# Performance work log

Hardware: AMD Instinct MI355X
Metric: run time of the kernel (lower is better)

## Reference

```python
import jax, jax.numpy as jnp
import numpy as np

B, ACT, C, H = 2048, 14, 128, 32
N = B * ACT                      # total nodes
E = B * ACT * ACT                # batched GCN edges
LOG_STD_MIN, LOG_STD_MAX = -20.0, 2.0


def setup_inputs() -> dict:
    key = jax.random.key(0)
    ks = jax.random.split(key, 8)
    def w(k, shape, fan_in):
        return jax.random.normal(k, shape, jnp.float32) / np.sqrt(fan_in).astype(np.float32)
    return {
        "state": jax.random.normal(ks[0], (N, C), jnp.float32),
        "conv_W": w(ks[1], (C, C), C),
        "conv_b": jnp.zeros((C,), jnp.float32),
        "lin1_W": w(ks[2], (2 * C, H), 2 * C),
        "lin1_b": jnp.zeros((H,), jnp.float32),
        "lin2_W": w(ks[3], (H, H), H),
        "lin2_b": jnp.zeros((H,), jnp.float32),
        "mu_W": w(ks[4], (H, 1), H),
        "mu_b": jnp.zeros((1,), jnp.float32),
        "sig_W": w(ks[5], (H, 1), H),
        "sig_b": jnp.zeros((1,), jnp.float32),
        "edge_index": jax.random.randint(ks[6], (2, E), 0, N, jnp.int32),
    }


def gcn_conv(x, W, b, src, dst):
    # PyG GCNConv default: add self-loops + symmetric normalization
    xw = x @ W                                           # [N, C]
    ones = jnp.ones(src.shape, x.dtype)
    deg = jax.ops.segment_sum(ones, dst, num_segments=N) + 1.0   # self-loop included
    dinv = jax.lax.rsqrt(deg)                            # deg^{-1/2}
    norm = dinv[src] * dinv[dst]                         # per-edge weight
    agg = jax.ops.segment_sum(xw[src] * norm[:, None], dst, num_segments=N)
    return agg + xw * (dinv * dinv)[:, None] + b         # self-loop term + bias


def reference(state, conv_W, conv_b, lin1_W, lin1_b, lin2_W, lin2_b,
              mu_W, mu_b, sig_W, sig_b, edge_index):
    src, dst = edge_index[0], edge_index[1]
    out = jax.nn.relu(gcn_conv(state, conv_W, conv_b, src, dst))
    x = (out + state).reshape(B, ACT, C)                 # [B, 14, C]
    # self.edges = all 196 directed pairs (i, j) over the 14-node graph
    e_src = jnp.repeat(jnp.arange(ACT), ACT)             # edges[:, 0]
    e_dst = jnp.tile(jnp.arange(ACT), ACT)               # edges[:, 1]
    ef = jnp.concatenate([x[:, e_src, :], x[:, e_dst, :]], axis=2)  # [B, 196, 2C]
    h = jax.nn.leaky_relu(ef @ lin1_W + lin1_b)          # slope 0.01 (torch default)
    h = jax.nn.leaky_relu(h @ lin2_W + lin2_b)           # [B, 196, H]
    log_std = jnp.clip(h @ sig_W + sig_b, LOG_STD_MIN, LOG_STD_MAX)
    std = jnp.exp(log_std)[..., 0]                       # [B, 196]
    mu = jax.nn.softplus(h @ mu_W + mu_b + 1e-10)[..., 0]  # [B, 196]
    # distribution parameters (return_D / deterministic paths)
    return jnp.stack([mu, std], axis=0)                  # [2, B, 196]
```

## Files before the change

kernel.cpp:

```cpp
#include <hip/hip_runtime.h>
#include <hip/hip_bf16.h>
#include <math.h>

#define NB    2048
#define ACT   14
#define NC    128
#define NH    32
#define NNODE (NB*ACT)
#define NEDGE (NB*ACT*ACT)
#define NPAIR (NB*ACT*ACT)
#define BCAP  64

__device__ __forceinline__ unsigned short f2bf(float f)
{
    unsigned u = __float_as_uint(f);
    return (unsigned short)((u + 0x7fff + ((u >> 16) & 1)) >> 16);
}
__device__ __forceinline__ float bfl(unsigned v) { return __uint_as_float(v << 16); }
__device__ __forceinline__ float bfh(unsigned v) { return __uint_as_float(v & 0xffff0000u); }

__global__ __launch_bounds__(256) void init_misc(
    int* __restrict__ cnt, unsigned short* __restrict__ ydummy,
    const float* __restrict__ W1, float* __restrict__ Wp)
{
    int idx = blockIdx.x * 256 + threadIdx.x;
    if (idx < NNODE) cnt[idx] = 0;
    if (idx < 128) ydummy[idx] = 0;
    if (idx < 128 * 64) {
        int k = idx >> 6, c = idx & 63;
        Wp[idx] = (c < 32) ? W1[k * 32 + c] : W1[(128 + k) * 32 + (c - 32)];
    }
}

__global__ void bucket_fill(const int* __restrict__ src, const int* __restrict__ dst,
                            int* __restrict__ cnt, int* __restrict__ bucket)
{
    int e = blockIdx.x * blockDim.x + threadIdx.x;
    if (e < NEDGE) {
        int d = dst[e];
        int slot = atomicAdd(&cnt[d], 1);
        if (slot < BCAP) bucket[(size_t)d * BCAP + slot] = src[e];
    }
}

__global__ __launch_bounds__(256) void gemm_k128_bf16(
    const float* __restrict__ A, const float* __restrict__ W,
    unsigned short* __restrict__ C, int ncols, const int* __restrict__ cnt)
{
    __shared__ float As[64 * 128];
    __shared__ float Ws[128 * 64];
    const int tid  = threadIdx.x;
    const int row0 = blockIdx.x * 64;
    const int col0 = blockIdx.y * 64;

    {
        const float4* Ag = (const float4*)(A + (size_t)row0 * 128);
#pragma unroll
        for (int it = 0; it < 8; ++it) {
            int idx = tid + it * 256;
            int r = idx >> 5;
            int c = (idx & 31) << 2;
            int cs = c ^ (((r >> 2) & 3) << 2);
            *((float4*)&As[r * 128 + cs]) = Ag[r * 32 + (c >> 2)];
        }
#pragma unroll
        for (int it = 0; it < 8; ++it) {
            int idx = tid + it * 256;
            int k = idx >> 4;
            int c = (idx & 15) << 2;
            *((float4*)&Ws[k * 64 + c]) =
                *((const float4*)&W[(size_t)k * ncols + col0 + c]);
        }
    }
    __syncthreads();

    const int tx = tid & 15;
    const int ty = tid >> 4;
    const int ri0 = ty * 4;

    float acc[4][4] = {};
    for (int k = 0; k < 128; k += 4) {
        float a_s[4][4];
        float w_s[4][4];
#pragma unroll
        for (int i = 0; i < 4; ++i) {
            int r = ri0 + i;
            *((float4*)&a_s[i][0]) =
                *((const float4*)&As[r * 128 + (k ^ (((r >> 2) & 3) << 2))]);
        }
#pragma unroll
        for (int kk = 0; kk < 4; ++kk) {
            *((float4*)&w_s[kk][0]) =
                *((const float4*)&Ws[(k + kk) * 64 + tx * 4]);
        }
#pragma unroll
        for (int kk = 0; kk < 4; ++kk)
#pragma unroll
            for (int i = 0; i < 4; ++i)
#pragma unroll
                for (int j = 0; j < 4; ++j)
                    acc[i][j] += a_s[i][kk] * w_s[kk][j];
    }

#pragma unroll
    for (int i = 0; i < 4; ++i) {
        float s = rsqrtf((float)cnt[row0 + ri0 + i] + 1.0f);
        ushort4 o;
        o.x = f2bf(acc[i][0] * s);
        o.y = f2bf(acc[i][1] * s);
        o.z = f2bf(acc[i][2] * s);
        o.w = f2bf(acc[i][3] * s);
        *((ushort4*)&C[(size_t)(row0 + ri0 + i) * ncols + col0 + tx * 4]) = o;
    }
}

__global__ __launch_bounds__(256) void gemm_k128(
    const float* __restrict__ A, const float* __restrict__ W,
    float* __restrict__ C, int ncols)
{
    __shared__ float As[64 * 128];
    __shared__ float Ws[128 * 64];
    const int tid  = threadIdx.x;
    const int row0 = blockIdx.x * 64;
    const int col0 = blockIdx.y * 64;

    {
        const float4* Ag = (const float4*)(A + (size_t)row0 * 128);
#pragma unroll
        for (int it = 0; it < 8; ++it) {
            int idx = tid + it * 256;
            int r = idx >> 5;
            int c = (idx & 31) << 2;
            int cs = c ^ (((r >> 2) & 3) << 2);
            *((float4*)&As[r * 128 + cs]) = Ag[r * 32 + (c >> 2)];
        }
#pragma unroll
        for (int it = 0; it < 8; ++it) {
            int idx = tid + it * 256;
            int k = idx >> 4;
            int c = (idx & 15) << 2;
            *((float4*)&Ws[k * 64 + c]) =
                *((const float4*)&W[(size_t)k * ncols + col0 + c]);
        }
    }
    __syncthreads();

    const int tx = tid & 15;
    const int ty = tid >> 4;
    const int ri0 = ty * 4;

    float acc[4][4] = {};
    for (int k = 0; k < 128; k += 4) {
        float a_s[4][4];
        float w_s[4][4];
#pragma unroll
        for (int i = 0; i < 4; ++i) {
            int r = ri0 + i;
            *((float4*)&a_s[i][0]) =
                *((const float4*)&As[r * 128 + (k ^ (((r >> 2) & 3) << 2))]);
        }
#pragma unroll
        for (int kk = 0; kk < 4; ++kk) {
            *((float4*)&w_s[kk][0]) =
                *((const float4*)&Ws[(k + kk) * 64 + tx * 4]);
        }
#pragma unroll
        for (int kk = 0; kk < 4; ++kk)
#pragma unroll
            for (int i = 0; i < 4; ++i)
#pragma unroll
                for (int j = 0; j < 4; ++j)
                    acc[i][j] += a_s[i][kk] * w_s[kk][j];
    }

#pragma unroll
    for (int i = 0; i < 4; ++i) {
        float4 v = make_float4(acc[i][0], acc[i][1], acc[i][2], acc[i][3]);
        *((float4*)&C[(size_t)(row0 + ri0 + i) * ncols + col0 + tx * 4]) = v;
    }
}

__global__ __launch_bounds__(256) void gather_agg(
    const int* __restrict__ bucket, const int* __restrict__ cnt,
    const unsigned short* __restrict__ y, const float* __restrict__ bias,
    const float* __restrict__ state, float* __restrict__ xout)
{
    const int lane = threadIdx.x & 31;
    const int d = (blockIdx.x * 256 + threadIdx.x) >> 5;
    if (d >= NNODE) return;

    const int c_true = cnt[d];
    const int c = c_true < BCAP ? c_true : BCAP;

    uint2 sv0 = ((const uint2*)(y + (size_t)d * NC))[lane];
    float4 acc;
    acc.x = bfl(sv0.x); acc.y = bfh(sv0.x);
    acc.z = bfl(sv0.y); acc.w = bfh(sv0.y);

    const int* brow = bucket + (size_t)d * BCAP;
    for (int base = 0; base < c; base += 32) {
        int rem = c - base;
        int m = rem < 32 ? rem : 32;
        int sv = (lane < m) ? brow[base + lane] : NNODE;
        int mm = (m + 3) & ~3;
        for (int j = 0; j < mm; j += 4) {
            int s0 = __shfl(sv, j + 0, 32);
            int s1 = __shfl(sv, j + 1, 32);
            int s2 = __shfl(sv, j + 2, 32);
            int s3 = __shfl(sv, j + 3, 32);
            uint2 a0 = ((const uint2*)(y + (size_t)s0 * NC))[lane];
            uint2 a1 = ((const uint2*)(y + (size_t)s1 * NC))[lane];
            uint2 a2 = ((const uint2*)(y + (size_t)s2 * NC))[lane];
            uint2 a3 = ((const uint2*)(y + (size_t)s3 * NC))[lane];
            acc.x += bfl(a0.x) + bfl(a1.x) + bfl(a2.x) + bfl(a3.x);
            acc.y += bfh(a0.x) + bfh(a1.x) + bfh(a2.x) + bfh(a3.x);
            acc.z += bfl(a0.y) + bfl(a1.y) + bfl(a2.y) + bfl(a3.y);
            acc.w += bfh(a0.y) + bfh(a1.y) + bfh(a2.y) + bfh(a3.y);
        }
    }

    const float dv = rsqrtf((float)c_true + 1.0f);
    float4 b  = ((const float4*)bias)[lane];
    float4 st = ((const float4*)(state + (size_t)d * NC))[lane];
    float4 r;
    r.x = fmaxf(acc.x * dv + b.x, 0.f) + st.x;
    r.y = fmaxf(acc.y * dv + b.y, 0.f) + st.y;
    r.z = fmaxf(acc.z * dv + b.z, 0.f) + st.z;
    r.w = fmaxf(acc.w * dv + b.w, 0.f) + st.w;
    ((float4*)(xout + (size_t)d * NC))[lane] = r;
}

__device__ __forceinline__ float softplusf(float z)
{
    return z > 0.f ? z + log1pf(expf(-z)) : log1pf(expf(z));
}

__global__ __launch_bounds__(256) void pairs_sgpr_kernel(
    const float* __restrict__ uv, const float* __restrict__ W2,
    const float* __restrict__ b1, const float* __restrict__ b2,
    const float* __restrict__ muW, const float* __restrict__ mu_b,
    const float* __restrict__ sigW, const float* __restrict__ sig_b,
    float* __restrict__ out)
{
    const int gid = blockIdx.x * 256 + threadIdx.x;
    const int b = gid / 196;
    const int p = gid - b * 196;
    const int i = p / 14;
    const int j = p - i * 14;

    const float* up = uv + (size_t)(b * ACT + i) * 64;
    const float* vp = uv + (size_t)(b * ACT + j) * 64 + 32;

    float h2[32];
#pragma unroll
    for (int l = 0; l < 32; ++l) h2[l] = b2[l];

#pragma unroll 2
    for (int k4 = 0; k4 < 8; ++k4) {
        float4 uu = ((const float4*)up)[k4];
        float4 vv = ((const float4*)vp)[k4];
#pragma unroll
        for (int kk = 0; kk < 4; ++kk) {
            float uvk = (kk == 0) ? uu.x + vv.x :
                        (kk == 1) ? uu.y + vv.y :
                        (kk == 2) ? uu.z + vv.z : uu.w + vv.w;
            float z = uvk + b1[k4 * 4 + kk];
            float h1k = z > 0.f ? z : 0.01f * z;
            const float* wrow = W2 + (k4 * 4 + kk) * 32;
#pragma unroll
            for (int l = 0; l < 32; ++l)
                h2[l] += h1k * wrow[l];
        }
    }

    float mu_acc = mu_b[0] + 1e-10f;
    float sg = sig_b[0];
#pragma unroll
    for (int l = 0; l < 32; ++l) {
        float h = h2[l];
        h = h > 0.f ? h : 0.01f * h;
        mu_acc += h * muW[l];
        sg += h * sigW[l];
    }
    out[gid]         = softplusf(mu_acc);
    out[NPAIR + gid] = expf(fminf(fmaxf(sg, -20.f), 2.f));
}

extern "C" void kernel_launch(void* const* d_in, const int* in_sizes, int n_in,
                              void* d_out, int out_size, void* d_ws, size_t ws_size,
                              hipStream_t stream)
{
    const float* state  = (const float*)d_in[0];
    const float* conv_W = (const float*)d_in[1];
    const float* conv_b = (const float*)d_in[2];
    const float* lin1_W = (const float*)d_in[3];
    const float* lin1_b = (const float*)d_in[4];
    const float* lin2_W = (const float*)d_in[5];
    const float* lin2_b = (const float*)d_in[6];
    const float* mu_W   = (const float*)d_in[7];
    const float* mu_b   = (const float*)d_in[8];
    const float* sig_W  = (const float*)d_in[9];
    const float* sig_b  = (const float*)d_in[10];
    const int*   eidx   = (const int*)d_in[11];
    const int* e_src = eidx;
    const int* e_dst = eidx + NEDGE;

    float* out = (float*)d_out;

    char* wsb = (char*)d_ws;
    unsigned short* y = (unsigned short*)wsb;
    char* p = wsb + (size_t)(NNODE + 1) * NC * sizeof(unsigned short);
    float* x = (float*)p;            p += (size_t)NNODE * NC * sizeof(float);
    int* cnt = (int*)p;              p += (size_t)NNODE * sizeof(int);
    int* bucket = (int*)p;           p += (size_t)NNODE * BCAP * sizeof(int);
    float* Wp = (float*)p;           p += 128 * 64 * sizeof(float);
    float* uvb = (float*)p;

    init_misc<<<(NNODE + 255) / 256, 256, 0, stream>>>(
        cnt, y + (size_t)NNODE * NC, lin1_W, Wp);

    bucket_fill<<<NEDGE / 256, 256, 0, stream>>>(e_src, e_dst, cnt, bucket);

    gemm_k128_bf16<<<dim3(NNODE / 64, 2), 256, 0, stream>>>(
        state, conv_W, y, 128, cnt);

    gather_agg<<<(NNODE * 32) / 256, 256, 0, stream>>>(
        bucket, cnt, y, conv_b, state, x);

    gemm_k128<<<dim3(NNODE / 64, 1), 256, 0, stream>>>(x, Wp, uvb, 64);

    pairs_sgpr_kernel<<<NPAIR / 256, 256, 0, stream>>>(
        uvb, lin2_W, lin1_b, lin2_b, mu_W, mu_b, sig_W, sig_b, out);
}
```

Baseline: 94.27 us.

## Compute pair-MLP second layer with bf16 MFMA instead of scalar FMAs

The per-pair 32x32 lin2 layer is rewritten so each wave processes 16 pairs with two 16x16x32 bf16 MFMA instructions, using a transposed bf16 copy of lin2_W built in the init kernel. Results go through shared memory, and 16 lanes per wave then finish the bias, leaky-relu and mu/sigma heads. This is meant to remove the heavy scalar FMA work of the old one-pair-per-thread kernel. In exchange, the first-layer activations and the weights are rounded to bf16, and three quarters of each wave sit idle during the epilogue.

```diff
diff --git a/kernel.cpp b/kernel.cpp
--- a/kernel.cpp
+++ b/kernel.cpp
@@ -11,6 +11,9 @@
 #define NPAIR (NB*ACT*ACT)
 #define BCAP  64
 
+typedef __attribute__((ext_vector_type(8))) short bf16x8;
+typedef __attribute__((ext_vector_type(4))) float f32x4;
+
 __device__ __forceinline__ unsigned short f2bf(float f)
 {
     unsigned u = __float_as_uint(f);
@@ -21,7 +24,8 @@
 
 __global__ __launch_bounds__(256) void init_misc(
     int* __restrict__ cnt, unsigned short* __restrict__ ydummy,
-    const float* __restrict__ W1, float* __restrict__ Wp)
+    const float* __restrict__ W1, float* __restrict__ Wp,
+    const float* __restrict__ W2, unsigned short* __restrict__ W2cm)
 {
     int idx = blockIdx.x * 256 + threadIdx.x;
     if (idx < NNODE) cnt[idx] = 0;
@@ -29,6 +33,10 @@
     if (idx < 128 * 64) {
         int k = idx >> 6, c = idx & 63;
         Wp[idx] = (c < 32) ? W1[k * 32 + c] : W1[(128 + k) * 32 + (c - 32)];
+    }
+    if (idx < 1024) {
+        int c = idx >> 5, kk = idx & 31;
+        W2cm[c * 32 + kk] = f2bf(W2[kk * 32 + c]);
     }
 }
 
@@ -235,55 +243,86 @@
     return z > 0.f ? z + log1pf(expf(-z)) : log1pf(expf(z));
 }
 
-__global__ __launch_bounds__(256) void pairs_sgpr_kernel(
-    const float* __restrict__ uv, const float* __restrict__ W2,
+__global__ __launch_bounds__(256) void pairs_mfma_kernel(
+    const float* __restrict__ uv, const unsigned short* __restrict__ W2cm,
     const float* __restrict__ b1, const float* __restrict__ b2,
     const float* __restrict__ muW, const float* __restrict__ mu_b,
     const float* __restrict__ sigW, const float* __restrict__ sig_b,
     float* __restrict__ out)
 {
-    const int gid = blockIdx.x * 256 + threadIdx.x;
-    const int b = gid / 196;
-    const int p = gid - b * 196;
+    __shared__ float h2s[4][16][36];
+    const int tid  = threadIdx.x;
+    const int wv   = tid >> 6;
+    const int lane = tid & 63;
+    const int lr   = lane & 15;
+    const int kb   = lane >> 4;
+    const int k0   = kb * 8;
+
+    const int tile = blockIdx.x * 4 + wv;
+    const int g = tile * 16 + lr;
+    const int b = g / 196;
+    const int p = g - b * 196;
     const int i = p / 14;
     const int j = p - i * 14;
 
-    const float* up = uv + (size_t)(b * ACT + i) * 64;
-    const float* vp = uv + (size_t)(b * ACT + j) * 64 + 32;
-
-    float h2[32];
-#pragma unroll
-    for (int l = 0; l < 32; ++l) h2[l] = b2[l];
-
-#pragma unroll 2
-    for (int k4 = 0; k4 < 8; ++k4) {
-        float4 uu = ((const float4*)up)[k4];
-        float4 vv = ((const float4*)vp)[k4];
-#pragma unroll
-        for (int kk = 0; kk < 4; ++kk) {
-            float uvk = (kk == 0) ? uu.x + vv.x :
-                        (kk == 1) ? uu.y + vv.y :
-                        (kk == 2) ? uu.z + vv.z : uu.w + vv.w;
-            float z = uvk + b1[k4 * 4 + kk];
-            float h1k = z > 0.f ? z : 0.01f * z;
-            const float* wrow = W2 + (k4 * 4 + kk) * 32;
-#pragma unroll
-            for (int l = 0; l < 32; ++l)
-                h2[l] += h1k * wrow[l];
-        }
-    }
-
-    float mu_acc = mu_b[0] + 1e-10f;
-    float sg = sig_b[0];
-#pragma unroll
-    for (int l = 0; l < 32; ++l) {
-        float h = h2[l];
-        h = h > 0.f ? h : 0.01f * h;
-        mu_acc += h * muW[l];
-        sg += h * sigW[l];
-    }
-    out[gid]         = softplusf(mu_acc);
-    out[NPAIR + gid] = expf(fminf(fmaxf(sg, -20.f), 2.f));
+    const float* up = uv + (size_t)(b * ACT + i) * 64 + k0;
+    const float* vp = uv + (size_t)(b * ACT + j) * 64 + 32 + k0;
+
+    float4 u0 = *((const float4*)up);
+    float4 u1 = *((const float4*)(up + 4));
+    float4 v0 = *((const float4*)vp);
+    float4 v1 = *((const float4*)(vp + 4));
+    float4 c0 = *((const float4*)(b1 + k0));
+    float4 c1 = *((const float4*)(b1 + k0 + 4));
+
+    float z[8];
+    z[0] = u0.x + v0.x + c0.x;  z[1] = u0.y + v0.y + c0.y;
+    z[2] = u0.z + v0.z + c0.z;  z[3] = u0.w + v0.w + c0.w;
+    z[4] = u1.x + v1.x + c1.x;  z[5] = u1.y + v1.y + c1.y;
+    z[6] = u1.z + v1.z + c1.z;  z[7] = u1.w + v1.w + c1.w;
+
+    bf16x8 a;
+#pragma unroll
+    for (int m = 0; m < 8; ++m) {
+        float h = z[m] > 0.f ? z[m] : 0.01f * z[m];
+        a[m] = (short)f2bf(h);
+    }
+
+    bf16x8 bf0 = *((const bf16x8*)(W2cm + (size_t)lr * 32 + k0));
+    bf16x8 bf1 = *((const bf16x8*)(W2cm + (size_t)(16 + lr) * 32 + k0));
+
+    f32x4 acc0 = {0.f, 0.f, 0.f, 0.f};
+    f32x4 acc1 = {0.f, 0.f, 0.f, 0.f};
+    acc0 = __builtin_amdgcn_mfma_f32_16x16x32_bf16(a, bf0, acc0, 0, 0, 0);
+    acc1 = __builtin_amdgcn_mfma_f32_16x16x32_bf16(a, bf1, acc1, 0, 0, 0);
+
+#pragma unroll
+    for (int t = 0; t < 4; ++t) {
+        h2s[wv][kb * 4 + t][lr]      = acc0[t];
+        h2s[wv][kb * 4 + t][16 + lr] = acc1[t];
+    }
+
+    if (lane < 16) {
+        const int row = lane;
+        const int gg = tile * 16 + row;
+        float mu_acc = mu_b[0] + 1e-10f;
+        float sg = sig_b[0];
+#pragma unroll
+        for (int l4 = 0; l4 < 8; ++l4) {
+            float4 hv = *((const float4*)&h2s[wv][row][l4 * 4]);
+            float hh[4] = {hv.x, hv.y, hv.z, hv.w};
+#pragma unroll
+            for (int t = 0; t < 4; ++t) {
+                int l = l4 * 4 + t;
+                float h = hh[t] + b2[l];
+                h = h > 0.f ? h : 0.01f * h;
+                mu_acc += h * muW[l];
+                sg     += h * sigW[l];
+            }
+        }
+        out[gg]         = softplusf(mu_acc);
+        out[NPAIR + gg] = expf(fminf(fmaxf(sg, -20.f), 2.f));
+    }
 }
 
 extern "C" void kernel_launch(void* const* d_in, const int* in_sizes, int n_in,
@@ -314,10 +353,11 @@
     int* cnt = (int*)p;              p += (size_t)NNODE * sizeof(int);
     int* bucket = (int*)p;           p += (size_t)NNODE * BCAP * sizeof(int);
     float* Wp = (float*)p;           p += 128 * 64 * sizeof(float);
+    unsigned short* W2cm = (unsigned short*)p;  p += 1024 * sizeof(unsigned short);
     float* uvb = (float*)p;
 
     init_misc<<<(NNODE + 255) / 256, 256, 0, stream>>>(
-        cnt, y + (size_t)NNODE * NC, lin1_W, Wp);
+        cnt, y + (size_t)NNODE * NC, lin1_W, Wp, lin2_W, W2cm);
 
     bucket_fill<<<NEDGE / 256, 256, 0, stream>>>(e_src, e_dst, cnt, bucket);
 
@@ -329,6 +369,6 @@
 
     gemm_k128<<<dim3(NNODE / 64, 1), 256, 0, stream>>>(x, Wp, uvb, 64);
 
-    pairs_sgpr_kernel<<<NPAIR / 256, 256, 0, stream>>>(
-        uvb, lin2_W, lin1_b, lin2_b, mu_W, mu_b, sig_W, sig_b, out);
-}
+    pairs_mfma_kernel<<<NPAIR / 16 / 4, 256, 0, stream>>>(
+        uvb, W2cm, lin1_b, lin2_b, mu_W, mu_b, sig_W, sig_b, out);
+}
```

New measurement: 100.8 us. 6.9% more time.

## Replace FP32 SIMT GEMMs with split-bf16 MFMA GEMMs

Applied to the files above, without the earlier changes.

Both node GEMMs (state@conv_W and x@lin1 projection) move from scalar FP32 FMA loops to MFMA 16x16x32 bf16 instructions. Activations are split into hi and lo bf16 parts, and weights are pre-converted and transposed in init_misc, so accuracy stays close to FP32 (2 products for gemm1, 3 for gemm2). This cuts the compute cost of the GEMM stages. It adds conversion work, larger LDS tiles and scalar bf16 stores on the output path.

```diff
diff --git a/kernel.cpp b/kernel.cpp
--- a/kernel.cpp
+++ b/kernel.cpp
@@ -11,24 +11,40 @@
 #define NPAIR (NB*ACT*ACT)
 #define BCAP  64
 
+typedef __attribute__((ext_vector_type(8))) short bf16x8;
+typedef __attribute__((ext_vector_type(4))) float f32x4;
+
 __device__ __forceinline__ unsigned short f2bf(float f)
 {
     unsigned u = __float_as_uint(f);
     return (unsigned short)((u + 0x7fff + ((u >> 16) & 1)) >> 16);
 }
+__device__ __forceinline__ float bf2f(unsigned short h)
+{
+    return __uint_as_float(((unsigned)h) << 16);
+}
 __device__ __forceinline__ float bfl(unsigned v) { return __uint_as_float(v << 16); }
 __device__ __forceinline__ float bfh(unsigned v) { return __uint_as_float(v & 0xffff0000u); }
 
 __global__ __launch_bounds__(256) void init_misc(
     int* __restrict__ cnt, unsigned short* __restrict__ ydummy,
-    const float* __restrict__ W1, float* __restrict__ Wp)
+    const float* __restrict__ convW, unsigned short* __restrict__ convWt,
+    const float* __restrict__ W1,
+    unsigned short* __restrict__ Whi, unsigned short* __restrict__ Wlo)
 {
     int idx = blockIdx.x * 256 + threadIdx.x;
     if (idx < NNODE) cnt[idx] = 0;
     if (idx < 128) ydummy[idx] = 0;
-    if (idx < 128 * 64) {
-        int k = idx >> 6, c = idx & 63;
-        Wp[idx] = (c < 32) ? W1[k * 32 + c] : W1[(128 + k) * 32 + (c - 32)];
+    if (idx < 128 * 128) {
+        int c = idx >> 7, k = idx & 127;
+        convWt[idx] = f2bf(convW[k * 128 + c]);
+    }
+    if (idx < 64 * 128) {
+        int c = idx >> 7, k = idx & 127;
+        float w = (c < 32) ? W1[k * 32 + c] : W1[(128 + k) * 32 + (c - 32)];
+        unsigned short h = f2bf(w);
+        Whi[idx] = h;
+        Wlo[idx] = f2bf(w - bf2f(h));
     }
 }
 
@@ -43,140 +59,155 @@
     }
 }
 
-__global__ __launch_bounds__(256) void gemm_k128_bf16(
-    const float* __restrict__ A, const float* __restrict__ W,
-    unsigned short* __restrict__ C, int ncols, const int* __restrict__ cnt)
-{
-    __shared__ float As[64 * 128];
-    __shared__ float Ws[128 * 64];
+__global__ __launch_bounds__(256) void gemm1_mfma(
+    const float* __restrict__ A, const unsigned short* __restrict__ Bt,
+    const int* __restrict__ cnt, unsigned short* __restrict__ y)
+{
+    __shared__ unsigned short Ah[128 * 128];
+    __shared__ unsigned short Alo[128 * 128];
+    __shared__ unsigned short Bl[128 * 128];
+    const int tid  = threadIdx.x;
+    const int row0 = blockIdx.x * 128;
+
+#pragma unroll
+    for (int it = 0; it < 16; ++it) {
+        int idx = tid + it * 256;
+        int r = idx >> 5;
+        int c = (idx & 31) << 2;
+        float4 v = ((const float4*)(A + (size_t)(row0 + r) * 128))[idx & 31];
+        ushort4 h, l;
+        h.x = f2bf(v.x); l.x = f2bf(v.x - bf2f(h.x));
+        h.y = f2bf(v.y); l.y = f2bf(v.y - bf2f(h.y));
+        h.z = f2bf(v.z); l.z = f2bf(v.z - bf2f(h.z));
+        h.w = f2bf(v.w); l.w = f2bf(v.w - bf2f(h.w));
+        int byte = (r * 256 + c * 2) ^ ((r & 7) << 4);
+        *(ushort4*)((char*)Ah  + byte) = h;
+        *(ushort4*)((char*)Alo + byte) = l;
+    }
+#pragma unroll
+    for (int it = 0; it < 8; ++it) {
+        int idx = tid + it * 256;
+        int cc = idx >> 4;
+        int kk = (idx & 15) << 3;
+        bf16x8 v = *((const bf16x8*)(Bt + cc * 128 + kk));
+        int byte = (cc * 256 + kk * 2) ^ ((cc & 7) << 4);
+        *(bf16x8*)((char*)Bl + byte) = v;
+    }
+    __syncthreads();
+
+    const int wv = tid >> 6, lane = tid & 63;
+    const int lr = lane & 15, kb = lane >> 4;
+    const int col0 = wv * 32;
+
+    f32x4 acc0[8], acc1[8];
+#pragma unroll
+    for (int mt = 0; mt < 8; ++mt) {
+        acc0[mt] = (f32x4){0.f, 0.f, 0.f, 0.f};
+        acc1[mt] = (f32x4){0.f, 0.f, 0.f, 0.f};
+    }
+
+#pragma unroll
+    for (int ks = 0; ks < 4; ++ks) {
+        const int kbyte = (ks * 32 + kb * 8) * 2;
+        int cb0 = ((col0 + lr) * 256 + kbyte) ^ (((col0 + lr) & 7) << 4);
+        int cb1 = ((col0 + 16 + lr) * 256 + kbyte) ^ (((col0 + 16 + lr) & 7) << 4);
+        bf16x8 b0 = *(const bf16x8*)((char*)Bl + cb0);
+        bf16x8 b1 = *(const bf16x8*)((char*)Bl + cb1);
+#pragma unroll
+        for (int mt = 0; mt < 8; ++mt) {
+            int rr = mt * 16 + lr;
+            int ab = (rr * 256 + kbyte) ^ ((rr & 7) << 4);
+            bf16x8 ah = *(const bf16x8*)((char*)Ah  + ab);
+            bf16x8 al = *(const bf16x8*)((char*)Alo + ab);
+            acc0[mt] = __builtin_amdgcn_mfma_f32_16x16x32_bf16(ah, b0, acc0[mt], 0, 0, 0);
+            acc0[mt] = __builtin_amdgcn_mfma_f32_16x16x32_bf16(al, b0, acc0[mt], 0, 0, 0);
+            acc1[mt] = __builtin_amdgcn_mfma_f32_16x16x32_bf16(ah, b1, acc1[mt], 0, 0, 0);
+            acc1[mt] = __builtin_amdgcn_mfma_f32_16x16x32_bf16(al, b1, acc1[mt], 0, 0, 0);
+        }
+    }
+
+#pragma unroll
+    for (int mt = 0; mt < 8; ++mt) {
+#pragma unroll
+        for (int t = 0; t < 4; ++t) {
+            int grow = row0 + mt * 16 + kb * 4 + t;
+            float s = rsqrtf((float)cnt[grow] + 1.0f);
+            y[(size_t)grow * 128 + col0 + lr]      = f2bf(acc0[mt][t] * s);
+            y[(size_t)grow * 128 + col0 + 16 + lr] = f2bf(acc1[mt][t] * s);
+        }
+    }
+}
+
+__global__ __launch_bounds__(256) void gemm2_mfma(
+    const float* __restrict__ X, const unsigned short* __restrict__ Whi,
+    const unsigned short* __restrict__ Wlo, float* __restrict__ U)
+{
+    __shared__ unsigned short Ah[64 * 128];
+    __shared__ unsigned short Alo[64 * 128];
+    __shared__ unsigned short Bh[64 * 128];
+    __shared__ unsigned short Blo[64 * 128];
     const int tid  = threadIdx.x;
     const int row0 = blockIdx.x * 64;
-    const int col0 = blockIdx.y * 64;
-
-    {
-        const float4* Ag = (const float4*)(A + (size_t)row0 * 128);
-#pragma unroll
-        for (int it = 0; it < 8; ++it) {
-            int idx = tid + it * 256;
-            int r = idx >> 5;
-            int c = (idx & 31) << 2;
-            int cs = c ^ (((r >> 2) & 3) << 2);
-            *((float4*)&As[r * 128 + cs]) = Ag[r * 32 + (c >> 2)];
-        }
-#pragma unroll
-        for (int it = 0; it < 8; ++it) {
-            int idx = tid + it * 256;
-            int k = idx >> 4;
-            int c = (idx & 15) << 2;
-            *((float4*)&Ws[k * 64 + c]) =
-                *((const float4*)&W[(size_t)k * ncols + col0 + c]);
-        }
+
+#pragma unroll
+    for (int it = 0; it < 8; ++it) {
+        int idx = tid + it * 256;
+        int r = idx >> 5;
+        int c = (idx & 31) << 2;
+        float4 v = ((const float4*)(X + (size_t)(row0 + r) * 128))[idx & 31];
+        ushort4 h, l;
+        h.x = f2bf(v.x); l.x = f2bf(v.x - bf2f(h.x));
+        h.y = f2bf(v.y); l.y = f2bf(v.y - bf2f(h.y));
+        h.z = f2bf(v.z); l.z = f2bf(v.z - bf2f(h.z));
+        h.w = f2bf(v.w); l.w = f2bf(v.w - bf2f(h.w));
+        int byte = (r * 256 + c * 2) ^ ((r & 7) << 4);
+        *(ushort4*)((char*)Ah  + byte) = h;
+        *(ushort4*)((char*)Alo + byte) = l;
+    }
+#pragma unroll
+    for (int it = 0; it < 4; ++it) {
+        int idx = tid + it * 256;
+        int cc = idx >> 4;
+        int kk = (idx & 15) << 3;
+        int byte = (cc * 256 + kk * 2) ^ ((cc & 7) << 4);
+        *(bf16x8*)((char*)Bh  + byte) = *((const bf16x8*)(Whi + cc * 128 + kk));
+        *(bf16x8*)((char*)Blo + byte) = *((const bf16x8*)(Wlo + cc * 128 + kk));
     }
     __syncthreads();
 
-    const int tx = tid & 15;
-    const int ty = tid >> 4;
-    const int ri0 = ty * 4;
-
-    float acc[4][4] = {};
-    for (int k = 0; k < 128; k += 4) {
-        float a_s[4][4];
-        float w_s[4][4];
-#pragma unroll
-        for (int i = 0; i < 4; ++i) {
-            int r = ri0 + i;
-            *((float4*)&a_s[i][0]) =
-                *((const float4*)&As[r * 128 + (k ^ (((r >> 2) & 3) << 2))]);
-        }
-#pragma unroll
-        for (int kk = 0; kk < 4; ++kk) {
-            *((float4*)&w_s[kk][0]) =
-                *((const float4*)&Ws[(k + kk) * 64 + tx * 4]);
-        }
-#pragma unroll
-        for (int kk = 0; kk < 4; ++kk)
-#pragma unroll
-            for (int i = 0; i < 4; ++i)
-#pragma unroll
-                for (int j = 0; j < 4; ++j)
-                    acc[i][j] += a_s[i][kk] * w_s[kk][j];
-    }
-
-#pragma unroll
-    for (int i = 0; i < 4; ++i) {
-        float s = rsqrtf((float)cnt[row0 + ri0 + i] + 1.0f);
-        ushort4 o;
-        o.x = f2bf(acc[i][0] * s);
-        o.y = f2bf(acc[i][1] * s);
-        o.z = f2bf(acc[i][2] * s);
-        o.w = f2bf(acc[i][3] * s);
-        *((ushort4*)&C[(size_t)(row0 + ri0 + i) * ncols + col0 + tx * 4]) = o;
-    }
-}
-
-__global__ __launch_bounds__(256) void gemm_k128(
-    const float* __restrict__ A, const float* __restrict__ W,
-    float* __restrict__ C, int ncols)
-{
-    __shared__ float As[64 * 128];
-    __shared__ float Ws[128 * 64];
-    const int tid  = threadIdx.x;
-    const int row0 = blockIdx.x * 64;
-    const int col0 = blockIdx.y * 64;
-
-    {
-        const float4* Ag = (const float4*)(A + (size_t)row0 * 128);
-#pragma unroll
-        for (int it = 0; it < 8; ++it) {
-            int idx = tid + it * 256;
-            int r = idx >> 5;
-            int c = (idx & 31) << 2;
-            int cs = c ^ (((r >> 2) & 3) << 2);
-            *((float4*)&As[r * 128 + cs]) = Ag[r * 32 + (c >> 2)];
-        }
-#pragma unroll
-        for (int it = 0; it < 8; ++it) {
-            int idx = tid + it * 256;
-            int k = idx >> 4;
-            int c = (idx & 15) << 2;
-            *((float4*)&Ws[k * 64 + c]) =
-                *((const float4*)&W[(size_t)k * ncols + col0 + c]);
-        }
-    }
-    __syncthreads();
-
-    const int tx = tid & 15;
-    const int ty = tid >> 4;
-    const int ri0 = ty * 4;
-
-    float acc[4][4] = {};
-    for (int k = 0; k < 128; k += 4) {
-        float a_s[4][4];
-        float w_s[4][4];
-#pragma unroll
-        for (int i = 0; i < 4; ++i) {
-            int r = ri0 + i;
-            *((float4*)&a_s[i][0]) =
-                *((const float4*)&As[r * 128 + (k ^ (((r >> 2) & 3) << 2))]);
-        }
-#pragma unroll
-        for (int kk = 0; kk < 4; ++kk) {
-            *((float4*)&w_s[kk][0]) =
-                *((const float4*)&Ws[(k + kk) * 64 + tx * 4]);
-        }
-#pragma unroll
-        for (int kk = 0; kk < 4; ++kk)
-#pragma unroll
-            for (int i = 0; i < 4; ++i)
-#pragma unroll
-                for (int j = 0; j < 4; ++j)
-                    acc[i][j] += a_s[i][kk] * w_s[kk][j];
-    }
-
-#pragma unroll
-    for (int i = 0; i < 4; ++i) {
-        float4 v = make_float4(acc[i][0], acc[i][1], acc[i][2], acc[i][3]);
-        *((float4*)&C[(size_t)(row0 + ri0 + i) * ncols + col0 + tx * 4]) = v;
+    const int wv = tid >> 6, lane = tid & 63;
+    const int lr = lane & 15, kb = lane >> 4;
+    const int col0 = wv * 16;
+
+    f32x4 acc[4];
+#pragma unroll
+    for (int mt = 0; mt < 4; ++mt) acc[mt] = (f32x4){0.f, 0.f, 0.f, 0.f};
+
+#pragma unroll
+    for (int ks = 0; ks < 4; ++ks) {
+        const int kbyte = (ks * 32 + kb * 8) * 2;
+        int cb = ((col0 + lr) * 256 + kbyte) ^ (((col0 + lr) & 7) << 4);
+        bf16x8 bh = *(const bf16x8*)((char*)Bh  + cb);
+        bf16x8 bl = *(const bf16x8*)((char*)Blo + cb);
+#pragma unroll
+        for (int mt = 0; mt < 4; ++mt) {
+            int rr = mt * 16 + lr;
+            int ab = (rr * 256 + kbyte) ^ ((rr & 7) << 4);
+            bf16x8 ah = *(const bf16x8*)((char*)Ah  + ab);
+            bf16x8 al = *(const bf16x8*)((char*)Alo + ab);
+            acc[mt] = __builtin_amdgcn_mfma_f32_16x16x32_bf16(ah, bh, acc[mt], 0, 0, 0);
+            acc[mt] = __builtin_amdgcn_mfma_f32_16x16x32_bf16(al, bh, acc[mt], 0, 0, 0);
+            acc[mt] = __builtin_amdgcn_mfma_f32_16x16x32_bf16(ah, bl, acc[mt], 0, 0, 0);
+        }
+    }
+
+#pragma unroll
+    for (int mt = 0; mt < 4; ++mt) {
+#pragma unroll
+        for (int t = 0; t < 4; ++t) {
+            int grow = row0 + mt * 16 + kb * 4 + t;
+            U[(size_t)grow * 64 + col0 + lr] = acc[mt][t];
+        }
     }
 }
 
@@ -313,21 +344,22 @@
     float* x = (float*)p;            p += (size_t)NNODE * NC * sizeof(float);
     int* cnt = (int*)p;              p += (size_t)NNODE * sizeof(int);
     int* bucket = (int*)p;           p += (size_t)NNODE * BCAP * sizeof(int);
-    float* Wp = (float*)p;           p += 128 * 64 * sizeof(float);
+    unsigned short* convWt = (unsigned short*)p;  p += 128 * 128 * sizeof(unsigned short);
+    unsigned short* Whi = (unsigned short*)p;     p += 64 * 128 * sizeof(unsigned short);
+    unsigned short* Wlo = (unsigned short*)p;     p += 64 * 128 * sizeof(unsigned short);
     float* uvb = (float*)p;
 
     init_misc<<<(NNODE + 255) / 256, 256, 0, stream>>>(
-        cnt, y + (size_t)NNODE * NC, lin1_W, Wp);
+        cnt, y + (size_t)NNODE * NC, conv_W, convWt, lin1_W, Whi, Wlo);
 
     bucket_fill<<<NEDGE / 256, 256, 0, stream>>>(e_src, e_dst, cnt, bucket);
 
-    gemm_k128_bf16<<<dim3(NNODE / 64, 2), 256, 0, stream>>>(
-        state, conv_W, y, 128, cnt);
+    gemm1_mfma<<<NNODE / 128, 256, 0, stream>>>(state, convWt, cnt, y);
 
     gather_agg<<<(NNODE * 32) / 256, 256, 0, stream>>>(
         bucket, cnt, y, conv_b, state, x);
 
-    gemm_k128<<<dim3(NNODE / 64, 1), 256, 0, stream>>>(x, Wp, uvb, 64);
+    gemm2_mfma<<<NNODE / 64, 256, 0, stream>>>(x, Whi, Wlo, uvb);
 
     pairs_sgpr_kernel<<<NPAIR / 256, 256, 0, stream>>>(
         uvb, lin2_W, lin1_b, lin2_b, mu_W, mu_b, sig_W, sig_b, out);
```

Measured after the change: 81.27 us. -13.8%, faster.
